# Performance work log

Hardware: AMD Instinct MI355X
Metric: run time of the kernel (lower is better)

The kernel has to match this reference:

```python
import jax, jax.numpy as jnp
import numpy as np

C, F, CLS, B, HW = 2048, 512, 200, 128, 14
SCALES = (4, 5, 7, 11)
EPS = 1e-5

def _pool_matrix(n, k):
    # PyTorch AdaptiveAvgPool2d bin edges: [floor(i*n/k), ceil((i+1)*n/k))
    P = np.zeros((k, n), np.float32)
    for i in range(k):
        s = (i * n) // k
        e = -((-(i + 1) * n) // k)
        P[i, s:e] = 1.0 / (e - s)
    return jnp.asarray(P)

_PMATS = [_pool_matrix(HW, k) for k in SCALES]

def _bn(x, g, b):
    # BatchNorm with batch statistics (train-mode), biased variance, eps=1e-5
    m = x.mean(0)
    v = x.var(0)
    return (x - m) * jax.lax.rsqrt(v + EPS) * g + b

def _head(h, g1, b1, w1, bi1, g2, b2, w2, bi2):
    # Sequential(BN, Linear, BN, ELU, Linear)
    h = _bn(h, g1, b1) @ w1.T + bi1
    h = jax.nn.elu(_bn(h, g2, b2))
    return h @ w2.T + bi2

def setup_inputs():
    key = jax.random.key(0)
    ks = iter(jax.random.split(key, 16))
    def rn(shape, scale=0.02):
        return jax.random.normal(next(ks), shape, jnp.float32) * scale
    d = {"x": jax.random.normal(next(ks), (B, C, HW, HW), jnp.float32)}
    d.update(g_bn_g=jnp.ones((C,)), g_bn_b=jnp.zeros((C,)), g_w=rn((4, C)), g_b=jnp.zeros((4,)))
    d.update(e_w=rn((C, C)), e_b=jnp.zeros((C,)), e_g=jnp.ones((C,)), e_bb=jnp.zeros((C,)))
    def head(p, din, dh):
        d[p + "_g1"] = jnp.ones((din,)); d[p + "_b1"] = jnp.zeros((din,))
        d[p + "_w1"] = rn((dh, din));   d[p + "_bi1"] = jnp.zeros((dh,))
        d[p + "_g2"] = jnp.ones((dh,)); d[p + "_b2"] = jnp.zeros((dh,))
        d[p + "_w2"] = rn((CLS, dh));   d[p + "_bi2"] = jnp.zeros((CLS,))
    head("hl", C, F)
    head("hh", C, F)
    head("hf", 2 * C, 2 * F)
    return d

def reference(x, g_bn_g, g_bn_b, g_w, g_b, e_w, e_b, e_g, e_bb,
              hl_g1, hl_b1, hl_w1, hl_bi1, hl_g2, hl_b2, hl_w2, hl_bi2,
              hh_g1, hh_b1, hh_w1, hh_bi1, hh_g2, hh_b2, hh_w2, hh_bi2,
              hf_g1, hf_b1, hf_w1, hf_bi1, hf_g2, hf_b2, hf_w2, hf_bi2):
    # Gate: global max pool -> BN -> ELU -> Linear -> hard gumbel-softmax (temp=1,
    # deterministic/eval: straight-through hard argmax over softmax)
    mp = x.max((2, 3))                                              # [B,C]
    logits = jax.nn.elu(_bn(mp, g_bn_g, g_bn_b)) @ g_w.T + g_b      # [B,4]
    soft = jax.nn.softmax(logits, -1)
    hard = jax.nn.one_hot(jnp.argmax(soft, -1), 4, dtype=soft.dtype)
    gw = jax.lax.stop_gradient(hard - soft) + soft                  # [B,4]
    # multi-scale adaptive avg pool (4,5,7,11) then global max per scale — fully batched
    ms = jnp.stack([jnp.einsum('ki,bcij,lj->bckl', P, x, P).max((2, 3)) for P in _PMATS], -1)  # [B,C,4]
    pool = jnp.einsum('bcs,bs->bc', ms, gw)                         # gated weighted sum
    # expert_low: 1x1 conv on 1x1 spatial == linear, then BN2d(batch stats) + ReLU
    xl = jax.nn.relu(_bn(pool @ e_w.T + e_b, e_g, e_bb))
    # NOTE: source computes expert_high(x) then overwrites with self.max(x) -> x_high = global max pool of x
    xh = mp
    xf = jnp.concatenate([xl, xh], -1)
    out_low = _head(xl, hl_g1, hl_b1, hl_w1, hl_bi1, hl_g2, hl_b2, hl_w2, hl_bi2)
    out_high = _head(xh, hh_g1, hh_b1, hh_w1, hh_bi1, hh_g2, hh_b2, hh_w2, hh_bi2)
    out = _head(xf, hf_g1, hf_b1, hf_w1, hf_bi1, hf_g2, hf_b2, hf_w2, hf_bi2)
    return (out_low, out_high, out)
```

## Files before the change

kernel.cpp:

```cpp
#include <hip/hip_runtime.h>
#include <math.h>

#define B_DIM 128
#define C_DIM 2048
#define HW2   196

typedef __attribute__((ext_vector_type(8))) short bf16x8;
typedef __attribute__((ext_vector_type(4))) float f32x4;

__device__ __forceinline__ unsigned short f2bf(float f) {
  unsigned u = __float_as_uint(f);
  u += 0x7FFFu + ((u >> 16) & 1u);
  return (unsigned short)(u >> 16);
}

__global__ __launch_bounds__(256) void pool_max_kernel(
    const float* __restrict__ x, float* __restrict__ mp, float* __restrict__ ms) {
  __shared__ float lds[4][4][208];
  const int tid  = threadIdx.x;
  const int w    = tid >> 6;
  const int lane = tid & 63;
  const int g    = lane >> 4;
  const int c    = lane & 15;
  const size_t waveBase = (size_t)blockIdx.x * 16 + w * 4;

  const float* src = x + waveBase * HW2;
  #pragma unroll
  for (int j = 0; j < 4; ++j) {
    int f = lane + 64 * j;
    if (f < 196) {
      int t = (f * 669) >> 15;
      float4 v = *(const float4*)(src + f * 4);
      *(float4*)&lds[w][t][(f - 49 * t) * 4] = v;
    }
  }

  float xv[14];
  const float* col = &lds[w][g][c];
  #pragma unroll
  for (int r = 0; r < 14; ++r) xv[r] = col[r * 14];

  float cmax = (c < 14) ? xv[0] : -INFINITY;
  #pragma unroll
  for (int r = 1; r < 14; ++r) if (c < 14) cmax = fmaxf(cmax, xv[r]);
  #pragma unroll
  for (int off = 8; off > 0; off >>= 1) cmax = fmaxf(cmax, __shfl_xor(cmax, off));

  float P[15];
  P[0] = 0.f;
  #pragma unroll
  for (int r = 0; r < 14; ++r) P[r + 1] = P[r] + xv[r];

  float sm0, sm1, sm2, sm3;

  {
    constexpr int rs[4] = {0, 3, 7, 10}, re[4] = {4, 7, 11, 14};
    const bool valid = (0x489u >> c) & 1;
    float vmax = -INFINITY;
    #pragma unroll
    for (int i = 0; i < 4; ++i) {
      float v  = P[re[i]] - P[rs[i]];
      float w2 = v + __shfl_down(v, 1);
      float w4 = w2 + __shfl_down(w2, 2);
      vmax = fmaxf(vmax, valid ? w4 : -INFINITY);
    }
    #pragma unroll
    for (int off = 8; off > 0; off >>= 1) vmax = fmaxf(vmax, __shfl_xor(vmax, off));
    sm0 = vmax * 0.0625f;
  }
  {
    constexpr int rs[5] = {0, 2, 5, 8, 11}, re[5] = {3, 6, 9, 12, 14};
    constexpr float srl[5] = {1.f/3.f, 0.25f, 0.25f, 0.25f, 1.f/3.f};
    const bool valid = (0x925u >> c) & 1;
    const bool is3   = (0x801u >> c) & 1;
    const float invc = is3 ? (1.f/3.f) : 0.25f;
    float vmax = -INFINITY;
    #pragma unroll
    for (int i = 0; i < 5; ++i) {
      float v  = P[re[i]] - P[rs[i]];
      float d1 = __shfl_down(v, 1);
      float d2 = __shfl_down(v, 2);
      float w2 = v + d1;
      float w3 = w2 + d2;
      float w4 = w2 + __shfl_down(w2, 2);
      float wv = (is3 ? w3 : w4) * invc * srl[i];
      vmax = fmaxf(vmax, valid ? wv : -INFINITY);
    }
    #pragma unroll
    for (int off = 8; off > 0; off >>= 1) vmax = fmaxf(vmax, __shfl_xor(vmax, off));
    sm1 = vmax;
  }
  {
    constexpr int rs[7] = {0, 2, 4, 6, 8, 10, 12};
    const bool valid = (0x1555u >> c) & 1;
    float vmax = -INFINITY;
    #pragma unroll
    for (int i = 0; i < 7; ++i) {
      float v  = P[rs[i] + 2] - P[rs[i]];
      float w2 = v + __shfl_down(v, 1);
      vmax = fmaxf(vmax, valid ? w2 : -INFINITY);
    }
    #pragma unroll
    for (int off = 8; off > 0; off >>= 1) vmax = fmaxf(vmax, __shfl_xor(vmax, off));
    sm2 = vmax * 0.25f;
  }
  {
    constexpr int rs[11] = {0, 1, 2, 3, 5, 6, 7, 8, 10, 11, 12};
    constexpr int re[11] = {2, 3, 4, 6, 7, 8, 9, 11, 12, 13, 14};
    constexpr float srl[11] = {0.5f, 0.5f, 0.5f, 1.f/3.f, 0.5f, 0.5f, 0.5f,
                               1.f/3.f, 0.5f, 0.5f, 0.5f};
    const bool valid = (0x1DEFu >> c) & 1;
    const bool is3   = (0x108u >> c) & 1;
    const float invc = is3 ? (1.f/3.f) : 0.5f;
    float vmax = -INFINITY;
    #pragma unroll
    for (int i = 0; i < 11; ++i) {
      float v  = P[re[i]] - P[rs[i]];
      float d1 = __shfl_down(v, 1);
      float d2 = __shfl_down(v, 2);
      float w2 = v + d1;
      float w3 = w2 + d2;
      float wv = (is3 ? w3 : w2) * invc * srl[i];
      vmax = fmaxf(vmax, valid ? wv : -INFINITY);
    }
    #pragma unroll
    for (int off = 8; off > 0; off >>= 1) vmax = fmaxf(vmax, __shfl_xor(vmax, off));
    sm3 = vmax;
  }

  if (c == 0) {
    size_t T = waveBase + g;
    mp[T] = cmax;
    *(float4*)&ms[T * 4] = make_float4(sm0, sm1, sm2, sm3);
  }
}

__global__ __launch_bounds__(256) void statsmp_kernel(
    const float* __restrict__ mp,
    const float* __restrict__ hh_g1, const float* __restrict__ hh_b1,
    const float* __restrict__ hf_g1, const float* __restrict__ hf_b1,
    float* __restrict__ mean_mp, float* __restrict__ rstd_mp,
    float* __restrict__ s_h, float* __restrict__ t_h,
    float* __restrict__ sf2, float* __restrict__ tf2) {
  const int ci = threadIdx.x & 15;
  const int g  = threadIdx.x >> 4;
  const int c  = blockIdx.x * 16 + ci;
  float s = 0.f, q = 0.f;
  #pragma unroll
  for (int r = 0; r < 8; ++r) {
    float v = mp[(size_t)(g * 8 + r) * C_DIM + c];
    s += v; q += v * v;
  }
  __shared__ float ss[16][16], qq[16][16];
  ss[g][ci] = s; qq[g][ci] = q;
  __syncthreads();
  if (g == 0) {
    float S = 0.f, Q = 0.f;
    #pragma unroll
    for (int j = 0; j < 16; ++j) { S += ss[j][ci]; Q += qq[j][ci]; }
    float m = S * (1.f / B_DIM);
    float var = Q * (1.f / B_DIM) - m * m;
    if (var < 0.f) var = 0.f;
    float r = rsqrtf(var + 1e-5f);
    mean_mp[c] = m; rstd_mp[c] = r;
    float a = r * hh_g1[c];        s_h[c] = a; t_h[c] = hh_b1[c] - m * a;
    float b = r * hf_g1[2048 + c]; sf2[c] = b; tf2[c] = hf_b1[2048 + c] - m * b;
  }
}

__global__ void gate_select_kernel(
    const float* __restrict__ mp,
    const float* __restrict__ mean, const float* __restrict__ rstd,
    const float* __restrict__ gg, const float* __restrict__ gb,
    const float* __restrict__ gw, const float* __restrict__ gbias,
    const float* __restrict__ ms, float* __restrict__ pool) {
  const int b = blockIdx.x;
  const int t = threadIdx.x;
  float s0 = 0.f, s1 = 0.f, s2 = 0.f, s3 = 0.f;
  for (int c = t; c < C_DIM; c += 256) {
    float v = mp[(size_t)b * C_DIM + c];
    float xn = (v - mean[c]) * rstd[c] * gg[c] + gb[c];
    float e = xn > 0.f ? xn : expm1f(xn);
    s0 += e * gw[c];
    s1 += e * gw[C_DIM + c];
    s2 += e * gw[2 * C_DIM + c];
    s3 += e * gw[3 * C_DIM + c];
  }
  __shared__ float red[4][256];
  __shared__ int ssel;
  red[0][t] = s0; red[1][t] = s1; red[2][t] = s2; red[3][t] = s3;
  __syncthreads();
  for (int st = 128; st > 0; st >>= 1) {
    if (t < st) {
      red[0][t] += red[0][t + st];
      red[1][t] += red[1][t + st];
      red[2][t] += red[2][t + st];
      red[3][t] += red[3][t + st];
    }
    __syncthreads();
  }
  if (t == 0) {
    float best = red[0][0] + gbias[0];
    int bi = 0;
    for (int j = 1; j < 4; ++j) {
      float l = red[j][0] + gbias[j];
      if (l > best) { best = l; bi = j; }
    }
    ssel = bi;
  }
  __syncthreads();
  const int sel = ssel;
  for (int c = t; c < C_DIM; c += 256)
    pool[(size_t)b * C_DIM + c] = ms[((size_t)b * C_DIM + c) * 4 + sel];
}

__global__ __launch_bounds__(256) void gemm_e_mfma_kernel(
    const float* __restrict__ A, const float* __restrict__ W,
    float* __restrict__ P) {
  __shared__ __align__(16) short As[128 * 64];
  __shared__ __align__(16) short Bs[64 * 64];
  const int t = threadIdx.x;
  const int n0 = blockIdx.x << 6;
  const int kbeg = blockIdx.y << 8;

  const int rowA = t >> 1, koffA = (t & 1) << 5;
  const int rowB = t >> 2, koffB = (t & 3) << 4;

  const int lane = t & 63, wav = t >> 6;
  const int r = lane & 15, kb = lane >> 4;
  int aoff[2][2], boff[2][4];
  #pragma unroll
  for (int kk = 0; kk < 2; ++kk) {
    #pragma unroll
    for (int mi = 0; mi < 2; ++mi) {
      int row = wav * 32 + mi * 16 + r;
      aoff[kk][mi] = row * 128 + ((((kk << 2) + kb) ^ (row & 7)) << 4);
    }
    #pragma unroll
    for (int ni = 0; ni < 4; ++ni) {
      int cl = ni * 16 + r;
      boff[kk][ni] = cl * 128 + ((((kk << 2) + kb) ^ (cl & 7)) << 4);
    }
  }

  f32x4 acc[2][4];
  #pragma unroll
  for (int mi = 0; mi < 2; ++mi)
    #pragma unroll
    for (int ni = 0; ni < 4; ++ni)
      acc[mi][ni] = (f32x4){0.f, 0.f, 0.f, 0.f};

  for (int kt = 0; kt < 256; kt += 64) {
    const int kg = kbeg + kt;
    const float4* ap = (const float4*)&A[(size_t)rowA * 2048 + kg + koffA];
    const float4* bp = (const float4*)&W[(size_t)(n0 + rowB) * 2048 + kg + koffB];
    float4 fa[8], fb[4];
    #pragma unroll
    for (int j = 0; j < 8; ++j) fa[j] = ap[j];
    #pragma unroll
    for (int j = 0; j < 4; ++j) fb[j] = bp[j];
    __syncthreads();
    #pragma unroll
    for (int j = 0; j < 4; ++j) {
      bf16x8 v;
      v[0] = (short)f2bf(fa[2*j].x);   v[1] = (short)f2bf(fa[2*j].y);
      v[2] = (short)f2bf(fa[2*j].z);   v[3] = (short)f2bf(fa[2*j].w);
      v[4] = (short)f2bf(fa[2*j+1].x); v[5] = (short)f2bf(fa[2*j+1].y);
      v[6] = (short)f2bf(fa[2*j+1].z); v[7] = (short)f2bf(fa[2*j+1].w);
      int slot = (koffA >> 3) + j;
      *(bf16x8*)((char*)As + rowA * 128 + ((slot ^ (rowA & 7)) << 4)) = v;
    }
    #pragma unroll
    for (int j = 0; j < 2; ++j) {
      bf16x8 v;
      v[0] = (short)f2bf(fb[2*j].x);   v[1] = (short)f2bf(fb[2*j].y);
      v[2] = (short)f2bf(fb[2*j].z);   v[3] = (short)f2bf(fb[2*j].w);
      v[4] = (short)f2bf(fb[2*j+1].x); v[5] = (short)f2bf(fb[2*j+1].y);
      v[6] = (short)f2bf(fb[2*j+1].z); v[7] = (short)f2bf(fb[2*j+1].w);
      int slot = (koffB >> 3) + j;
      *(bf16x8*)((char*)Bs + rowB * 128 + ((slot ^ (rowB & 7)) << 4)) = v;
    }
    __syncthreads();
    #pragma unroll
    for (int kk = 0; kk < 2; ++kk) {
      bf16x8 a0 = *(bf16x8*)((char*)As + aoff[kk][0]);
      bf16x8 a1 = *(bf16x8*)((char*)As + aoff[kk][1]);
      bf16x8 b0 = *(bf16x8*)((char*)Bs + boff[kk][0]);
      bf16x8 b1 = *(bf16x8*)((char*)Bs + boff[kk][1]);
      bf16x8 b2 = *(bf16x8*)((char*)Bs + boff[kk][2]);
      bf16x8 b3 = *(bf16x8*)((char*)Bs + boff[kk][3]);
      acc[0][0] = __builtin_amdgcn_mfma_f32_16x16x32_bf16(a0, b0, acc[0][0], 0, 0, 0);
      acc[0][1] = __builtin_amdgcn_mfma_f32_16x16x32_bf16(a0, b1, acc[0][1], 0, 0, 0);
      acc[0][2] = __builtin_amdgcn_mfma_f32_16x16x32_bf16(a0, b2, acc[0][2], 0, 0, 0);
      acc[0][3] = __builtin_amdgcn_mfma_f32_16x16x32_bf16(a0, b3, acc[0][3], 0, 0, 0);
      acc[1][0] = __builtin_amdgcn_mfma_f32_16x16x32_bf16(a1, b0, acc[1][0], 0, 0, 0);
      acc[1][1] = __builtin_amdgcn_mfma_f32_16x16x32_bf16(a1, b1, acc[1][1], 0, 0, 0);
      acc[1][2] = __builtin_amdgcn_mfma_f32_16x16x32_bf16(a1, b2, acc[1][2], 0, 0, 0);
      acc[1][3] = __builtin_amdgcn_mfma_f32_16x16x32_bf16(a1, b3, acc[1][3], 0, 0, 0);
    }
  }

  float* Pz = P + ((size_t)blockIdx.y << 18);
  #pragma unroll
  for (int mi = 0; mi < 2; ++mi) {
    int row = wav * 32 + mi * 16 + kb * 4;
    #pragma unroll
    for (int ni = 0; ni < 4; ++ni) {
      int cl = n0 + ni * 16 + r;
      #pragma unroll
      for (int g2 = 0; g2 < 4; ++g2)
        Pz[(size_t)(row + g2) * 2048 + cl] = acc[mi][ni][g2];
    }
  }
}

__global__ __launch_bounds__(256) void expert_fused_kernel(
    const float* __restrict__ Pe, const float* __restrict__ e_b,
    const float* __restrict__ e_g, const float* __restrict__ e_bb,
    const float* __restrict__ hl_g1, const float* __restrict__ hl_b1,
    const float* __restrict__ hf_g1, const float* __restrict__ hf_b1,
    float* __restrict__ xl,
    float* __restrict__ s_l, float* __restrict__ t_l,
    float* __restrict__ sf1, float* __restrict__ tf1) {
  const int ci = threadIdx.x & 15;
  const int g  = threadIdx.x >> 4;
  const int c  = blockIdx.x * 16 + ci;
  float v[8];
  float s = 0.f, q = 0.f;
  const float bias = e_b[c];
  #pragma unroll
  for (int r = 0; r < 8; ++r) {
    const size_t row = g * 8 + r;
    float acc = bias;
    #pragma unroll
    for (int z = 0; z < 8; ++z)
      acc += Pe[((size_t)z << 18) + row * 2048 + c];
    v[r] = acc; s += acc; q += acc * acc;
  }
  __shared__ float ss[16][16], qq[16][16];
  __shared__ float sm[16], sr[16];
  ss[g][ci] = s; qq[g][ci] = q;
  __syncthreads();
  if (g == 0) {
    float S = 0.f, Q = 0.f;
    #pragma unroll
    for (int j = 0; j < 16; ++j) { S += ss[j][ci]; Q += qq[j][ci]; }
    float m = S * (1.f / B_DIM);
    float var = Q * (1.f / B_DIM) - m * m;
    if (var < 0.f) var = 0.f;
    sm[ci] = m; sr[ci] = rsqrtf(var + 1e-5f);
  }
  __syncthreads();
  const float m = sm[ci], rst = sr[ci];
  const float eg = e_g[c], eb2 = e_bb[c];
  float s2 = 0.f, q2 = 0.f;
  #pragma unroll
  for (int r = 0; r < 8; ++r) {
    float xv = fmaxf((v[r] - m) * rst * eg + eb2, 0.f);
    xl[(size_t)(g * 8 + r) * 2048 + c] = xv;
    s2 += xv; q2 += xv * xv;
  }
  __syncthreads();
  ss[g][ci] = s2; qq[g][ci] = q2;
  __syncthreads();
  if (g == 0) {
    float S = 0.f, Q = 0.f;
    #pragma unroll
    for (int j = 0; j < 16; ++j) { S += ss[j][ci]; Q += qq[j][ci]; }
    float mm = S * (1.f / B_DIM);
    float var = Q * (1.f / B_DIM) - mm * mm;
    if (var < 0.f) var = 0.f;
    float rr = rsqrtf(var + 1e-5f);
    float a = rr * hl_g1[c]; s_l[c] = a; t_l[c] = hl_b1[c] - mm * a;
    float b = rr * hf_g1[c]; sf1[c] = b; tf1[c] = hf_b1[c] - mm * b;
  }
}

__global__ __launch_bounds__(256) void gemm_w1_mfma_kernel(
    const float* __restrict__ xl, const float* __restrict__ mp,
    const float* __restrict__ s_l, const float* __restrict__ t_l,
    const float* __restrict__ s_h, const float* __restrict__ t_h,
    const float* __restrict__ sf1, const float* __restrict__ tf1,
    const float* __restrict__ sf2, const float* __restrict__ tf2,
    const float* __restrict__ hl_w1, const float* __restrict__ hh_w1,
    const float* __restrict__ hf_w1,
    float* __restrict__ P_l, float* __restrict__ P_h, float* __restrict__ P_f) {
  __shared__ __align__(16) short As[128 * 64];
  __shared__ __align__(16) short Bs[64 * 64];
  const int jx = blockIdx.x;
  const int z  = blockIdx.y;
  const float *A, *S, *T, *Wt;
  float* P;
  int N, Kdim, n0, kA0, kW0, Kc;
  if (jx < 8) {
    N = 512; Kdim = 2048; Kc = 128; Wt = hl_w1; n0 = jx << 6;
    kW0 = z * 128; kA0 = kW0; A = xl; S = s_l; T = t_l;
    P = P_l + ((size_t)z << 16);
  } else if (jx < 16) {
    N = 512; Kdim = 2048; Kc = 128; Wt = hh_w1; n0 = (jx - 8) << 6;
    kW0 = z * 128; kA0 = kW0; A = mp; S = s_h; T = t_h;
    P = P_h + ((size_t)z << 16);
  } else {
    N = 1024; Kdim = 4096; Kc = 256; Wt = hf_w1; n0 = (jx - 16) << 6;
    kW0 = z * 256;
    if (kW0 >= 2048) { A = mp; S = sf2; T = tf2; kA0 = kW0 - 2048; }
    else             { A = xl; S = sf1; T = tf1; kA0 = kW0; }
    P = P_f + ((size_t)z << 17);
  }
  const int t = threadIdx.x;
  const int rowA = t >> 1, koffA = (t & 1) << 5;
  const int rowB = t >> 2, koffB = (t & 3) << 4;

  const int lane = t & 63, wav = t >> 6;
  const int r = lane & 15, kb = lane >> 4;
  int aoff[2][2], boff[2][4];
  #pragma unroll
  for (int kk = 0; kk < 2; ++kk) {
    #pragma unroll
    for (int mi = 0; mi < 2; ++mi) {
      int row = wav * 32 + mi * 16 + r;
      aoff[kk][mi] = row * 128 + ((((kk << 2) + kb) ^ (row & 7)) << 4);
    }
    #pragma unroll
    for (int ni = 0; ni < 4; ++ni) {
      int cl = ni * 16 + r;
      boff[kk][ni] = cl * 128 + ((((kk << 2) + kb) ^ (cl & 7)) << 4);
    }
  }

  f32x4 acc[2][4];
  #pragma unroll
  for (int mi = 0; mi < 2; ++mi)
    #pragma unroll
    for (int ni = 0; ni < 4; ++ni)
      acc[mi][ni] = (f32x4){0.f, 0.f, 0.f, 0.f};

  for (int kt = 0; kt < Kc; kt += 64) {
    const int ka = kA0 + kt + koffA;
    const float4* ap = (const float4*)&A[(size_t)rowA * 2048 + ka];
    const float4* sp = (const float4*)&S[ka];
    const float4* tp = (const float4*)&T[ka];
    const float4* bp = (const float4*)&Wt[(size_t)(n0 + rowB) * Kdim + kW0 + kt + koffB];
    float4 fa[8], fb[4];
    #pragma unroll
    for (int j = 0; j < 8; ++j) fa[j] = ap[j];
    #pragma unroll
    for (int j = 0; j < 8; ++j) {
      float4 s4 = sp[j], t4 = tp[j];
      fa[j].x = fmaf(fa[j].x, s4.x, t4.x);
      fa[j].y = fmaf(fa[j].y, s4.y, t4.y);
      fa[j].z = fmaf(fa[j].z, s4.z, t4.z);
      fa[j].w = fmaf(fa[j].w, s4.w, t4.w);
    }
    #pragma unroll
    for (int j = 0; j < 4; ++j) fb[j] = bp[j];
    __syncthreads();
    #pragma unroll
    for (int j = 0; j < 4; ++j) {
      bf16x8 v;
      v[0] = (short)f2bf(fa[2*j].x);   v[1] = (short)f2bf(fa[2*j].y);
      v[2] = (short)f2bf(fa[2*j].z);   v[3] = (short)f2bf(fa[2*j].w);
      v[4] = (short)f2bf(fa[2*j+1].x); v[5] = (short)f2bf(fa[2*j+1].y);
      v[6] = (short)f2bf(fa[2*j+1].z); v[7] = (short)f2bf(fa[2*j+1].w);
      int slot = (koffA >> 3) + j;
      *(bf16x8*)((char*)As + rowA * 128 + ((slot ^ (rowA & 7)) << 4)) = v;
    }
    #pragma unroll
    for (int j = 0; j < 2; ++j) {
      bf16x8 v;
      v[0] = (short)f2bf(fb[2*j].x);   v[1] = (short)f2bf(fb[2*j].y);
      v[2] = (short)f2bf(fb[2*j].z);   v[3] = (short)f2bf(fb[2*j].w);
      v[4] = (short)f2bf(fb[2*j+1].x); v[5] = (short)f2bf(fb[2*j+1].y);
      v[6] = (short)f2bf(fb[2*j+1].z); v[7] = (short)f2bf(fb[2*j+1].w);
      int slot = (koffB >> 3) + j;
      *(bf16x8*)((char*)Bs + rowB * 128 + ((slot ^ (rowB & 7)) << 4)) = v;
    }
    __syncthreads();
    #pragma unroll
    for (int kk = 0; kk < 2; ++kk) {
      bf16x8 a0 = *(bf16x8*)((char*)As + aoff[kk][0]);
      bf16x8 a1 = *(bf16x8*)((char*)As + aoff[kk][1]);
      bf16x8 b0 = *(bf16x8*)((char*)Bs + boff[kk][0]);
      bf16x8 b1 = *(bf16x8*)((char*)Bs + boff[kk][1]);
      bf16x8 b2 = *(bf16x8*)((char*)Bs + boff[kk][2]);
      bf16x8 b3 = *(bf16x8*)((char*)Bs + boff[kk][3]);
      acc[0][0] = __builtin_amdgcn_mfma_f32_16x16x32_bf16(a0, b0, acc[0][0], 0, 0, 0);
      acc[0][1] = __builtin_amdgcn_mfma_f32_16x16x32_bf16(a0, b1, acc[0][1], 0, 0, 0);
      acc[0][2] = __builtin_amdgcn_mfma_f32_16x16x32_bf16(a0, b2, acc[0][2], 0, 0, 0);
      acc[0][3] = __builtin_amdgcn_mfma_f32_16x16x32_bf16(a0, b3, acc[0][3], 0, 0, 0);
      acc[1][0] = __builtin_amdgcn_mfma_f32_16x16x32_bf16(a1, b0, acc[1][0], 0, 0, 0);
      acc[1][1] = __builtin_amdgcn_mfma_f32_16x16x32_bf16(a1, b1, acc[1][1], 0, 0, 0);
      acc[1][2] = __builtin_amdgcn_mfma_f32_16x16x32_bf16(a1, b2, acc[1][2], 0, 0, 0);
      acc[1][3] = __builtin_amdgcn_mfma_f32_16x16x32_bf16(a1, b3, acc[1][3], 0, 0, 0);
    }
  }

  #pragma unroll
  for (int mi = 0; mi < 2; ++mi) {
    int row = wav * 32 + mi * 16 + kb * 4;
    #pragma unroll
    for (int ni = 0; ni < 4; ++ni) {
      int cl = n0 + ni * 16 + r;
      #pragma unroll
      for (int g2 = 0; g2 < 4; ++g2)
        P[(size_t)(row + g2) * N + cl] = acc[mi][ni][g2];
    }
  }
}

__global__ __launch_bounds__(256) void heads_fused_kernel(
    const float* __restrict__ P_l, const float* __restrict__ P_h,
    const float* __restrict__ P_f,
    const float* __restrict__ bl1, const float* __restrict__ bh1,
    const float* __restrict__ bf1,
    const float* __restrict__ g2l, const float* __restrict__ b2l,
    const float* __restrict__ g2h, const float* __restrict__ b2h,
    const float* __restrict__ g2f, const float* __restrict__ b2f,
    float* __restrict__ a2_l, float* __restrict__ a2_h, float* __restrict__ a2_f) {
  const int ci = threadIdx.x & 15;
  const int g  = threadIdx.x >> 4;
  const int cj = blockIdx.x * 16 + ci;
  const float *P, *bi, *g2, *b2;
  float* out;
  int N, cc;
  if (cj < 512)       { P = P_l; bi = bl1; g2 = g2l; b2 = b2l; out = a2_l; N = 512;  cc = cj; }
  else if (cj < 1024) { P = P_h; bi = bh1; g2 = g2h; b2 = b2h; out = a2_h; N = 512;  cc = cj - 512; }
  else                { P = P_f; bi = bf1; g2 = g2f; b2 = b2f; out = a2_f; N = 1024; cc = cj - 1024; }
  const size_t sstride = (size_t)N * 128;
  float v[8];
  float s = 0.f, q = 0.f;
  const float bias = bi[cc];
  #pragma unroll
  for (int r = 0; r < 8; ++r) {
    const size_t row = g * 8 + r;
    float acc = bias;
    #pragma unroll
    for (int z = 0; z < 16; ++z)
      acc += P[(size_t)z * sstride + row * N + cc];
    v[r] = acc; s += acc; q += acc * acc;
  }
  __shared__ float ss[16][16], qq[16][16];
  __shared__ float sm[16], sr[16];
  ss[g][ci] = s; qq[g][ci] = q;
  __syncthreads();
  if (g == 0) {
    float S = 0.f, Q = 0.f;
    #pragma unroll
    for (int j = 0; j < 16; ++j) { S += ss[j][ci]; Q += qq[j][ci]; }
    float m = S * (1.f / B_DIM);
    float var = Q * (1.f / B_DIM) - m * m;
    if (var < 0.f) var = 0.f;
    sm[ci] = m; sr[ci] = rsqrtf(var + 1e-5f);
  }
  __syncthreads();
  const float m = sm[ci], rr = sr[ci];
  const float gg = g2[cc], bb = b2[cc];
  #pragma unroll
  for (int r = 0; r < 8; ++r) {
    float xn = (v[r] - m) * rr * gg + bb;
    out[(size_t)(g * 8 + r) * N + cc] = xn > 0.f ? xn : expm1f(xn);
  }
}

__global__ __launch_bounds__(256) void gemm_w2_kernel(
    const float* __restrict__ a2_l, const float* __restrict__ a2_h,
    const float* __restrict__ a2_f,
    const float* __restrict__ hl_w2, const float* __restrict__ hh_w2,
    const float* __restrict__ hf_w2,
    float* __restrict__ Pw) {
  const int jx = blockIdx.x;
  const int z  = blockIdx.z;
  const float *A, *Wt;
  int K, Kc, pOff, n0;
  if (jx < 4)      { A = a2_l; Wt = hl_w2; K = 512;  Kc = 64;  pOff = 0;     n0 = jx << 6; }
  else if (jx < 8) { A = a2_h; Wt = hh_w2; K = 512;  Kc = 64;  pOff = 25600; n0 = (jx - 4) << 6; }
  else             { A = a2_f; Wt = hf_w2; K = 1024; Kc = 128; pOff = 51200; n0 = (jx - 8) << 6; }
  const int kbeg = z * Kc;
  const int m0 = blockIdx.y << 6;
  __shared__ float As[32][68];
  __shared__ float Bs[32][68];
  const int t = threadIdx.x;
  const int lr = t >> 3;
  const int lk4 = (t & 7) << 2;
  const int tx = t & 15, ty = t >> 4;
  float acc[4][4] = {{0.f}};
  const float4 z4 = make_float4(0.f, 0.f, 0.f, 0.f);
  for (int k0 = kbeg; k0 < kbeg + Kc; k0 += 32) {
    float4 a0 = *(const float4*)&A[(size_t)(m0 + lr) * K + k0 + lk4];
    float4 a1 = *(const float4*)&A[(size_t)(m0 + lr + 32) * K + k0 + lk4];
    int n1 = n0 + lr, n2 = n0 + lr + 32;
    float4 b0 = (n1 < 200) ? *(const float4*)&Wt[(size_t)n1 * K + k0 + lk4] : z4;
    float4 b1 = (n2 < 200) ? *(const float4*)&Wt[(size_t)n2 * K + k0 + lk4] : z4;
    __syncthreads();
    As[lk4 + 0][lr] = a0.x; As[lk4 + 1][lr] = a0.y; As[lk4 + 2][lr] = a0.z; As[lk4 + 3][lr] = a0.w;
    As[lk4 + 0][lr + 32] = a1.x; As[lk4 + 1][lr + 32] = a1.y; As[lk4 + 2][lr + 32] = a1.z; As[lk4 + 3][lr + 32] = a1.w;
    Bs[lk4 + 0][lr] = b0.x; Bs[lk4 + 1][lr] = b0.y; Bs[lk4 + 2][lr] = b0.z; Bs[lk4 + 3][lr] = b0.w;
    Bs[lk4 + 0][lr + 32] = b1.x; Bs[lk4 + 1][lr + 32] = b1.y; Bs[lk4 + 2][lr + 32] = b1.z; Bs[lk4 + 3][lr + 32] = b1.w;
    __syncthreads();
    #pragma unroll
    for (int kk = 0; kk < 32; ++kk) {
      float4 av = *(const float4*)&As[kk][ty << 2];
      float4 bv = *(const float4*)&Bs[kk][tx << 2];
      acc[0][0] = fmaf(av.x, bv.x, acc[0][0]); acc[0][1] = fmaf(av.x, bv.y, acc[0][1]);
      acc[0][2] = fmaf(av.x, bv.z, acc[0][2]); acc[0][3] = fmaf(av.x, bv.w, acc[0][3]);
      acc[1][0] = fmaf(av.y, bv.x, acc[1][0]); acc[1][1] = fmaf(av.y, bv.y, acc[1][1]);
      acc[1][2] = fmaf(av.y, bv.z, acc[1][2]); acc[1][3] = fmaf(av.y, bv.w, acc[1][3]);
      acc[2][0] = fmaf(av.z, bv.x, acc[2][0]); acc[2][1] = fmaf(av.z, bv.y, acc[2][1]);
      acc[2][2] = fmaf(av.z, bv.z, acc[2][2]); acc[2][3] = fmaf(av.z, bv.w, acc[2][3]);
      acc[3][0] = fmaf(av.w, bv.x, acc[3][0]); acc[3][1] = fmaf(av.w, bv.y, acc[3][1]);
      acc[3][2] = fmaf(av.w, bv.z, acc[3][2]); acc[3][3] = fmaf(av.w, bv.w, acc[3][3]);
    }
  }
  float* Pz = Pw + (size_t)z * 76800 + pOff;
  #pragma unroll
  for (int i = 0; i < 4; ++i) {
    int m = m0 + (ty << 2) + i;
    #pragma unroll
    for (int j = 0; j < 4; ++j) {
      int n = n0 + (tx << 2) + j;
      if (n < 200) Pz[(size_t)m * 200 + n] = acc[i][j];
    }
  }
}

__global__ void reduce_out_kernel(const float* __restrict__ P,
                                  const float* __restrict__ bl,
                                  const float* __restrict__ bh,
                                  const float* __restrict__ bf,
                                  float* __restrict__ out) {
  int i = blockIdx.x * 256 + threadIdx.x;
  if (i >= 76800) return;
  int job = i / 25600;
  int n = (i - job * 25600) % 200;
  float s = (job == 0) ? bl[n] : (job == 1) ? bh[n] : bf[n];
  for (int z = 0; z < 8; ++z) s += P[(size_t)z * 76800 + i];
  out[i] = s;
}

extern "C" void kernel_launch(void* const* d_in, const int* in_sizes, int n_in,
                              void* d_out, int out_size, void* d_ws, size_t ws_size,
                              hipStream_t stream) {
  const float* x      = (const float*)d_in[0];
  const float* g_bn_g = (const float*)d_in[1];
  const float* g_bn_b = (const float*)d_in[2];
  const float* g_w    = (const float*)d_in[3];
  const float* g_b    = (const float*)d_in[4];
  const float* e_w    = (const float*)d_in[5];
  const float* e_b    = (const float*)d_in[6];
  const float* e_g    = (const float*)d_in[7];
  const float* e_bb   = (const float*)d_in[8];
  const float* hl_g1  = (const float*)d_in[9];
  const float* hl_b1  = (const float*)d_in[10];
  const float* hl_w1  = (const float*)d_in[11];
  const float* hl_bi1 = (const float*)d_in[12];
  const float* hl_g2  = (const float*)d_in[13];
  const float* hl_b2  = (const float*)d_in[14];
  const float* hl_w2  = (const float*)d_in[15];
  const float* hl_bi2 = (const float*)d_in[16];
  const float* hh_g1  = (const float*)d_in[17];
  const float* hh_b1  = (const float*)d_in[18];
  const float* hh_w1  = (const float*)d_in[19];
  const float* hh_bi1 = (const float*)d_in[20];
  const float* hh_g2  = (const float*)d_in[21];
  const float* hh_b2  = (const float*)d_in[22];
  const float* hh_w2  = (const float*)d_in[23];
  const float* hh_bi2 = (const float*)d_in[24];
  const float* hf_g1  = (const float*)d_in[25];
  const float* hf_b1  = (const float*)d_in[26];
  const float* hf_w1  = (const float*)d_in[27];
  const float* hf_bi1 = (const float*)d_in[28];
  const float* hf_g2  = (const float*)d_in[29];
  const float* hf_b2  = (const float*)d_in[30];
  const float* hf_w2  = (const float*)d_in[31];
  const float* hf_bi2 = (const float*)d_in[32];
  float* out = (float*)d_out;

  float* W = (float*)d_ws;
  const size_t BC = (size_t)B_DIM * C_DIM;
  float* mp   = W;
  float* ms   = mp + BC;
  float* pool = ms + BC * 4;
  float* xl   = pool + BC;
  float* a2_l = xl + BC;
  float* a2_h = a2_l + 128 * 512;
  float* a2_f = a2_h + 128 * 512;
  float* st   = a2_f + 128 * 1024;
  float* mean_mp = st;           float* rstd_mp = st + 2048;
  float* s_h  = st + 2 * 2048;   float* t_h  = st + 3 * 2048;
  float* sf2  = st + 4 * 2048;   float* tf2  = st + 5 * 2048;
  float* s_l  = st + 6 * 2048;   float* t_l  = st + 7 * 2048;
  float* sf1  = st + 8 * 2048;   float* tf1  = st + 9 * 2048;
  float* P_e  = st + 10 * 2048;
  float* P_l2 = P_e + 8 * BC;
  float* P_hh = P_l2 + (size_t)16 * 65536;
  float* P_f  = P_hh + (size_t)16 * 65536;
  float* P_w2 = P_e;

  pool_max_kernel<<<16384, 256, 0, stream>>>(x, mp, ms);

  statsmp_kernel<<<128, 256, 0, stream>>>(mp, hh_g1, hh_b1, hf_g1, hf_b1,
                                          mean_mp, rstd_mp, s_h, t_h, sf2, tf2);

  gate_select_kernel<<<128, 256, 0, stream>>>(mp, mean_mp, rstd_mp, g_bn_g, g_bn_b,
                                              g_w, g_b, ms, pool);

  gemm_e_mfma_kernel<<<dim3(32, 8), 256, 0, stream>>>(pool, e_w, P_e);

  expert_fused_kernel<<<128, 256, 0, stream>>>(P_e, e_b, e_g, e_bb,
                                               hl_g1, hl_b1, hf_g1, hf_b1,
                                               xl, s_l, t_l, sf1, tf1);

  gemm_w1_mfma_kernel<<<dim3(32, 16), 256, 0, stream>>>(
      xl, mp, s_l, t_l, s_h, t_h, sf1, tf1, sf2, tf2,
      hl_w1, hh_w1, hf_w1, P_l2, P_hh, P_f);

  heads_fused_kernel<<<128, 256, 0, stream>>>(
      P_l2, P_hh, P_f, hl_bi1, hh_bi1, hf_bi1,
      hl_g2, hl_b2, hh_g2, hh_b2, hf_g2, hf_b2,
      a2_l, a2_h, a2_f);

  gemm_w2_kernel<<<dim3(12, 2, 8), 256, 0, stream>>>(
      a2_l, a2_h, a2_f, hl_w2, hh_w2, hf_w2, P_w2);

  reduce_out_kernel<<<300, 256, 0, stream>>>(P_w2, hl_bi2, hh_bi2, hf_bi2, out);
}
```

Baseline: 139.5 us.

## Use MFMA for final head GEMM, drop split-K reduce, halve W1 split-K

```diff
diff --git a/kernel.cpp b/kernel.cpp
--- a/kernel.cpp
+++ b/kernel.cpp
@@ -30,8 +30,8 @@
     int f = lane + 64 * j;
     if (f < 196) {
       int t = (f * 669) >> 15;
-      float4 v = *(const float4*)(src + f * 4);
-      *(float4*)&lds[w][t][(f - 49 * t) * 4] = v;
+      f32x4 v = __builtin_nontemporal_load((const f32x4*)(src + f * 4));
+      *(f32x4*)&lds[w][t][(f - 49 * t) * 4] = v;
     }
   }
 
@@ -393,16 +393,16 @@
   float* P;
   int N, Kdim, n0, kA0, kW0, Kc;
   if (jx < 8) {
-    N = 512; Kdim = 2048; Kc = 128; Wt = hl_w1; n0 = jx << 6;
-    kW0 = z * 128; kA0 = kW0; A = xl; S = s_l; T = t_l;
+    N = 512; Kdim = 2048; Kc = 256; Wt = hl_w1; n0 = jx << 6;
+    kW0 = z * 256; kA0 = kW0; A = xl; S = s_l; T = t_l;
     P = P_l + ((size_t)z << 16);
   } else if (jx < 16) {
-    N = 512; Kdim = 2048; Kc = 128; Wt = hh_w1; n0 = (jx - 8) << 6;
-    kW0 = z * 128; kA0 = kW0; A = mp; S = s_h; T = t_h;
+    N = 512; Kdim = 2048; Kc = 256; Wt = hh_w1; n0 = (jx - 8) << 6;
+    kW0 = z * 256; kA0 = kW0; A = mp; S = s_h; T = t_h;
     P = P_h + ((size_t)z << 16);
   } else {
-    N = 1024; Kdim = 4096; Kc = 256; Wt = hf_w1; n0 = (jx - 16) << 6;
-    kW0 = z * 256;
+    N = 1024; Kdim = 4096; Kc = 512; Wt = hf_w1; n0 = (jx - 16) << 6;
+    kW0 = z * 512;
     if (kW0 >= 2048) { A = mp; S = sf2; T = tf2; kA0 = kW0 - 2048; }
     else             { A = xl; S = sf1; T = tf1; kA0 = kW0; }
     P = P_f + ((size_t)z << 17);
@@ -535,7 +535,7 @@
     const size_t row = g * 8 + r;
     float acc = bias;
     #pragma unroll
-    for (int z = 0; z < 16; ++z)
+    for (int z = 0; z < 8; ++z)
       acc += P[(size_t)z * sstride + row * N + cc];
     v[r] = acc; s += acc; q += acc * acc;
   }
@@ -562,79 +562,123 @@
   }
 }
 
-__global__ __launch_bounds__(256) void gemm_w2_kernel(
+__global__ __launch_bounds__(256) void gemm_w2_mfma_kernel(
     const float* __restrict__ a2_l, const float* __restrict__ a2_h,
     const float* __restrict__ a2_f,
     const float* __restrict__ hl_w2, const float* __restrict__ hh_w2,
     const float* __restrict__ hf_w2,
-    float* __restrict__ Pw) {
+    const float* __restrict__ bl2, const float* __restrict__ bh2,
+    const float* __restrict__ bf2,
+    float* __restrict__ out) {
+  __shared__ __align__(16) short As[128 * 64];
+  __shared__ __align__(16) short Bs[64 * 64];
   const int jx = blockIdx.x;
-  const int z  = blockIdx.z;
-  const float *A, *Wt;
-  int K, Kc, pOff, n0;
-  if (jx < 4)      { A = a2_l; Wt = hl_w2; K = 512;  Kc = 64;  pOff = 0;     n0 = jx << 6; }
-  else if (jx < 8) { A = a2_h; Wt = hh_w2; K = 512;  Kc = 64;  pOff = 25600; n0 = (jx - 4) << 6; }
-  else             { A = a2_f; Wt = hf_w2; K = 1024; Kc = 128; pOff = 51200; n0 = (jx - 8) << 6; }
-  const int kbeg = z * Kc;
-  const int m0 = blockIdx.y << 6;
-  __shared__ float As[32][68];
-  __shared__ float Bs[32][68];
+  const float *A, *Wt, *bi;
+  int K, outOff;
+  if (jx < 4)      { A = a2_l; Wt = hl_w2; bi = bl2; K = 512;  outOff = 0; }
+  else if (jx < 8) { A = a2_h; Wt = hh_w2; bi = bh2; K = 512;  outOff = 25600; }
+  else             { A = a2_f; Wt = hf_w2; bi = bf2; K = 1024; outOff = 51200; }
+  const int n0 = (jx & 3) << 6;
+
   const int t = threadIdx.x;
-  const int lr = t >> 3;
-  const int lk4 = (t & 7) << 2;
-  const int tx = t & 15, ty = t >> 4;
-  float acc[4][4] = {{0.f}};
+  const int rowA = t >> 1, koffA = (t & 1) << 5;
+  const int rowB = t >> 2, koffB = (t & 3) << 4;
+
+  const int lane = t & 63, wav = t >> 6;
+  const int r = lane & 15, kb = lane >> 4;
+  int aoff[2][2], boff[2][4];
+  #pragma unroll
+  for (int kk = 0; kk < 2; ++kk) {
+    #pragma unroll
+    for (int mi = 0; mi < 2; ++mi) {
+      int row = wav * 32 + mi * 16 + r;
+      aoff[kk][mi] = row * 128 + ((((kk << 2) + kb) ^ (row & 7)) << 4);
+    }
+    #pragma unroll
+    for (int ni = 0; ni < 4; ++ni) {
+      int cl = ni * 16 + r;
+      boff[kk][ni] = cl * 128 + ((((kk << 2) + kb) ^ (cl & 7)) << 4);
+    }
+  }
+
+  f32x4 acc[2][4];
+  #pragma unroll
+  for (int mi = 0; mi < 2; ++mi)
+    #pragma unroll
+    for (int ni = 0; ni < 4; ++ni)
+      acc[mi][ni] = (f32x4){0.f, 0.f, 0.f, 0.f};
+
+  const int wrow = n0 + rowB;
   const float4 z4 = make_float4(0.f, 0.f, 0.f, 0.f);
-  for (int k0 = kbeg; k0 < kbeg + Kc; k0 += 32) {
-    float4 a0 = *(const float4*)&A[(size_t)(m0 + lr) * K + k0 + lk4];
-    float4 a1 = *(const float4*)&A[(size_t)(m0 + lr + 32) * K + k0 + lk4];
-    int n1 = n0 + lr, n2 = n0 + lr + 32;
-    float4 b0 = (n1 < 200) ? *(const float4*)&Wt[(size_t)n1 * K + k0 + lk4] : z4;
-    float4 b1 = (n2 < 200) ? *(const float4*)&Wt[(size_t)n2 * K + k0 + lk4] : z4;
+  for (int kt = 0; kt < K; kt += 64) {
+    const float4* ap = (const float4*)&A[(size_t)rowA * K + kt + koffA];
+    float4 fa[8], fb[4];
+    #pragma unroll
+    for (int j = 0; j < 8; ++j) fa[j] = ap[j];
+    if (wrow < 200) {
+      const float4* bp = (const float4*)&Wt[(size_t)wrow * K + kt + koffB];
+      #pragma unroll
+      for (int j = 0; j < 4; ++j) fb[j] = bp[j];
+    } else {
+      #pragma unroll
+      for (int j = 0; j < 4; ++j) fb[j] = z4;
+    }
     __syncthreads();
-    As[lk4 + 0][lr] = a0.x; As[lk4 + 1][lr] = a0.y; As[lk4 + 2][lr] = a0.z; As[lk4 + 3][lr] = a0.w;
-    As[lk4 + 0][lr + 32] = a1.x; As[lk4 + 1][lr + 32] = a1.y; As[lk4 + 2][lr + 32] = a1.z; As[lk4 + 3][lr + 32] = a1.w;
-    Bs[lk4 + 0][lr] = b0.x; Bs[lk4 + 1][lr] = b0.y; Bs[lk4 + 2][lr] = b0.z; Bs[lk4 + 3][lr] = b0.w;
-    Bs[lk4 + 0][lr + 32] = b1.x; Bs[lk4 + 1][lr + 32] = b1.y; Bs[lk4 + 2][lr + 32] = b1.z; Bs[lk4 + 3][lr + 32] = b1.w;
+    #pragma unroll
+    for (int j = 0; j < 4; ++j) {
+      bf16x8 v;
+      v[0] = (short)f2bf(fa[2*j].x);   v[1] = (short)f2bf(fa[2*j].y);
+      v[2] = (short)f2bf(fa[2*j].z);   v[3] = (short)f2bf(fa[2*j].w);
+      v[4] = (short)f2bf(fa[2*j+1].x); v[5] = (short)f2bf(fa[2*j+1].y);
+      v[6] = (short)f2bf(fa[2*j+1].z); v[7] = (short)f2bf(fa[2*j+1].w);
+      int slot = (koffA >> 3) + j;
+      *(bf16x8*)((char*)As + rowA * 128 + ((slot ^ (rowA & 7)) << 4)) = v;
+    }
+    #pragma unroll
+    for (int j = 0; j < 2; ++j) {
+      bf16x8 v;
+      v[0] = (short)f2bf(fb[2*j].x);   v[1] = (short)f2bf(fb[2*j].y);
+      v[2] = (short)f2bf(fb[2*j].z);   v[3] = (short)f2bf(fb[2*j].w);
+      v[4] = (short)f2bf(fb[2*j+1].x); v[5] = (short)f2bf(fb[2*j+1].y);
+      v[6] = (short)f2bf(fb[2*j+1].z); v[7] = (short)f2bf(fb[2*j+1].w);
+      int slot = (koffB >> 3) + j;
+      *(bf16x8*)((char*)Bs + rowB * 128 + ((slot ^ (rowB & 7)) << 4)) = v;
+    }
     __syncthreads();
     #pragma unroll
-    for (int kk = 0; kk < 32; ++kk) {
-      float4 av = *(const float4*)&As[kk][ty << 2];
-      float4 bv = *(const float4*)&Bs[kk][tx << 2];
-      acc[0][0] = fmaf(av.x, bv.x, acc[0][0]); acc[0][1] = fmaf(av.x, bv.y, acc[0][1]);
-      acc[0][2] = fmaf(av.x, bv.z, acc[0][2]); acc[0][3] = fmaf(av.x, bv.w, acc[0][3]);
-      acc[1][0] = fmaf(av.y, bv.x, acc[1][0]); acc[1][1] = fmaf(av.y, bv.y, acc[1][1]);
-      acc[1][2] = fmaf(av.y, bv.z, acc[1][2]); acc[1][3] = fmaf(av.y, bv.w, acc[1][3]);
-      acc[2][0] = fmaf(av.z, bv.x, acc[2][0]); acc[2][1] = fmaf(av.z, bv.y, acc[2][1]);
-      acc[2][2] = fmaf(av.z, bv.z, acc[2][2]); acc[2][3] = fmaf(av.z, bv.w, acc[2][3]);
-      acc[3][0] = fmaf(av.w, bv.x, acc[3][0]); acc[3][1] = fmaf(av.w, bv.y, acc[3][1]);
-      acc[3][2] = fmaf(av.w, bv.z, acc[3][2]); acc[3][3] = fmaf(av.w, bv.w, acc[3][3]);
-    }
-  }
-  float* Pz = Pw + (size_t)z * 76800 + pOff;
-  #pragma unroll
-  for (int i = 0; i < 4; ++i) {
-    int m = m0 + (ty << 2) + i;
-    #pragma unroll
-    for (int j = 0; j < 4; ++j) {
-      int n = n0 + (tx << 2) + j;
-      if (n < 200) Pz[(size_t)m * 200 + n] = acc[i][j];
-    }
-  }
-}
-
-__global__ void reduce_out_kernel(const float* __restrict__ P,
-                                  const float* __restrict__ bl,
-                                  const float* __restrict__ bh,
-                                  const float* __restrict__ bf,
-                                  float* __restrict__ out) {
-  int i = blockIdx.x * 256 + threadIdx.x;
-  if (i >= 76800) return;
-  int job = i / 25600;
-  int n = (i - job * 25600) % 200;
-  float s = (job == 0) ? bl[n] : (job == 1) ? bh[n] : bf[n];
-  for (int z = 0; z < 8; ++z) s += P[(size_t)z * 76800 + i];
-  out[i] = s;
+    for (int kk = 0; kk < 2; ++kk) {
+      bf16x8 a0 = *(bf16x8*)((char*)As + aoff[kk][0]);
+      bf16x8 a1 = *(bf16x8*)((char*)As + aoff[kk][1]);
+      bf16x8 b0 = *(bf16x8*)((char*)Bs + boff[kk][0]);
+      bf16x8 b1 = *(bf16x8*)((char*)Bs + boff[kk][1]);
+      bf16x8 b2 = *(bf16x8*)((char*)Bs + boff[kk][2]);
+      bf16x8 b3 = *(bf16x8*)((char*)Bs + boff[kk][3]);
+      acc[0][0] = __builtin_amdgcn_mfma_f32_16x16x32_bf16(a0, b0, acc[0][0], 0, 0, 0);
+      acc[0][1] = __builtin_amdgcn_mfma_f32_16x16x32_bf16(a0, b1, acc[0][1], 0, 0, 0);
+      acc[0][2] = __builtin_amdgcn_mfma_f32_16x16x32_bf16(a0, b2, acc[0][2], 0, 0, 0);
+      acc[0][3] = __builtin_amdgcn_mfma_f32_16x16x32_bf16(a0, b3, acc[0][3], 0, 0, 0);
+      acc[1][0] = __builtin_amdgcn_mfma_f32_16x16x32_bf16(a1, b0, acc[1][0], 0, 0, 0);
+      acc[1][1] = __builtin_amdgcn_mfma_f32_16x16x32_bf16(a1, b1, acc[1][1], 0, 0, 0);
+      acc[1][2] = __builtin_amdgcn_mfma_f32_16x16x32_bf16(a1, b2, acc[1][2], 0, 0, 0);
+      acc[1][3] = __builtin_amdgcn_mfma_f32_16x16x32_bf16(a1, b3, acc[1][3], 0, 0, 0);
+    }
+  }
+
+  float* O = out + outOff;
+  #pragma unroll
+  for (int mi = 0; mi < 2; ++mi) {
+    int row = wav * 32 + mi * 16 + kb * 4;
+    #pragma unroll
+    for (int ni = 0; ni < 4; ++ni) {
+      int cl = n0 + ni * 16 + r;
+      if (cl < 200) {
+        float bv = bi[cl];
+        #pragma unroll
+        for (int g2 = 0; g2 < 4; ++g2)
+          O[(size_t)(row + g2) * 200 + cl] = acc[mi][ni][g2] + bv;
+      }
+    }
+  }
 }
 
 extern "C" void kernel_launch(void* const* d_in, const int* in_sizes, int n_in,
@@ -692,9 +736,8 @@
   float* sf1  = st + 8 * 2048;   float* tf1  = st + 9 * 2048;
   float* P_e  = st + 10 * 2048;
   float* P_l2 = P_e + 8 * BC;
-  float* P_hh = P_l2 + (size_t)16 * 65536;
-  float* P_f  = P_hh + (size_t)16 * 65536;
-  float* P_w2 = P_e;
+  float* P_hh = P_l2 + (size_t)8 * 65536;
+  float* P_f  = P_hh + (size_t)8 * 65536;
 
   pool_max_kernel<<<16384, 256, 0, stream>>>(x, mp, ms);
 
@@ -710,7 +753,7 @@
                                                hl_g1, hl_b1, hf_g1, hf_b1,
                                                xl, s_l, t_l, sf1, tf1);
 
-  gemm_w1_mfma_kernel<<<dim3(32, 16), 256, 0, stream>>>(
+  gemm_w1_mfma_kernel<<<dim3(32, 8), 256, 0, stream>>>(
       xl, mp, s_l, t_l, s_h, t_h, sf1, tf1, sf2, tf2,
       hl_w1, hh_w1, hf_w1, P_l2, P_hh, P_f);
 
@@ -719,8 +762,7 @@
       hl_g2, hl_b2, hh_g2, hh_b2, hf_g2, hf_b2,
       a2_l, a2_h, a2_f);
 
-  gemm_w2_kernel<<<dim3(12, 2, 8), 256, 0, stream>>>(
-      a2_l, a2_h, a2_f, hl_w2, hh_w2, hf_w2, P_w2);
-
-  reduce_out_kernel<<<300, 256, 0, stream>>>(P_w2, hl_bi2, hh_bi2, hf_bi2, out);
-}
+  gemm_w2_mfma_kernel<<<12, 256, 0, stream>>>(
+      a2_l, a2_h, a2_f, hl_w2, hh_w2, hf_w2,
+      hl_bi2, hh_bi2, hf_bi2, out);
+}
```

Measured after the change: 157.2 us. 12.7% more time.

## Retile first-layer head GEMM to 64-row M tiles with halved split-K

Applied to the files above, without the earlier changes.

```diff
diff --git a/kernel.cpp b/kernel.cpp
--- a/kernel.cpp
+++ b/kernel.cpp
@@ -385,42 +385,39 @@
     const float* __restrict__ hl_w1, const float* __restrict__ hh_w1,
     const float* __restrict__ hf_w1,
     float* __restrict__ P_l, float* __restrict__ P_h, float* __restrict__ P_f) {
-  __shared__ __align__(16) short As[128 * 64];
+  __shared__ __align__(16) short As[64 * 64];
   __shared__ __align__(16) short Bs[64 * 64];
   const int jx = blockIdx.x;
-  const int z  = blockIdx.y;
+  const int m0 = blockIdx.y << 6;
+  const int z  = blockIdx.z;
   const float *A, *S, *T, *Wt;
   float* P;
   int N, Kdim, n0, kA0, kW0, Kc;
   if (jx < 8) {
-    N = 512; Kdim = 2048; Kc = 128; Wt = hl_w1; n0 = jx << 6;
-    kW0 = z * 128; kA0 = kW0; A = xl; S = s_l; T = t_l;
+    N = 512; Kdim = 2048; Kc = 256; Wt = hl_w1; n0 = jx << 6;
+    kW0 = z * 256; kA0 = kW0; A = xl; S = s_l; T = t_l;
     P = P_l + ((size_t)z << 16);
   } else if (jx < 16) {
-    N = 512; Kdim = 2048; Kc = 128; Wt = hh_w1; n0 = (jx - 8) << 6;
-    kW0 = z * 128; kA0 = kW0; A = mp; S = s_h; T = t_h;
+    N = 512; Kdim = 2048; Kc = 256; Wt = hh_w1; n0 = (jx - 8) << 6;
+    kW0 = z * 256; kA0 = kW0; A = mp; S = s_h; T = t_h;
     P = P_h + ((size_t)z << 16);
   } else {
-    N = 1024; Kdim = 4096; Kc = 256; Wt = hf_w1; n0 = (jx - 16) << 6;
-    kW0 = z * 256;
+    N = 1024; Kdim = 4096; Kc = 512; Wt = hf_w1; n0 = (jx - 16) << 6;
+    kW0 = z * 512;
     if (kW0 >= 2048) { A = mp; S = sf2; T = tf2; kA0 = kW0 - 2048; }
     else             { A = xl; S = sf1; T = tf1; kA0 = kW0; }
     P = P_f + ((size_t)z << 17);
   }
   const int t = threadIdx.x;
-  const int rowA = t >> 1, koffA = (t & 1) << 5;
-  const int rowB = t >> 2, koffB = (t & 3) << 4;
+  const int rowS = t >> 2, koff = (t & 3) << 4;
 
   const int lane = t & 63, wav = t >> 6;
   const int r = lane & 15, kb = lane >> 4;
-  int aoff[2][2], boff[2][4];
+  int aoff[2], boff[2][4];
   #pragma unroll
   for (int kk = 0; kk < 2; ++kk) {
-    #pragma unroll
-    for (int mi = 0; mi < 2; ++mi) {
-      int row = wav * 32 + mi * 16 + r;
-      aoff[kk][mi] = row * 128 + ((((kk << 2) + kb) ^ (row & 7)) << 4);
-    }
+    int row = wav * 16 + r;
+    aoff[kk] = row * 128 + ((((kk << 2) + kb) ^ (row & 7)) << 4);
     #pragma unroll
     for (int ni = 0; ni < 4; ++ni) {
       int cl = ni * 16 + r;
@@ -428,24 +425,21 @@
     }
   }
 
-  f32x4 acc[2][4];
-  #pragma unroll
-  for (int mi = 0; mi < 2; ++mi)
-    #pragma unroll
-    for (int ni = 0; ni < 4; ++ni)
-      acc[mi][ni] = (f32x4){0.f, 0.f, 0.f, 0.f};
+  f32x4 acc[4];
+  #pragma unroll
+  for (int ni = 0; ni < 4; ++ni) acc[ni] = (f32x4){0.f, 0.f, 0.f, 0.f};
 
   for (int kt = 0; kt < Kc; kt += 64) {
-    const int ka = kA0 + kt + koffA;
-    const float4* ap = (const float4*)&A[(size_t)rowA * 2048 + ka];
+    const int ka = kA0 + kt + koff;
+    const float4* ap = (const float4*)&A[(size_t)(m0 + rowS) * 2048 + ka];
     const float4* sp = (const float4*)&S[ka];
     const float4* tp = (const float4*)&T[ka];
-    const float4* bp = (const float4*)&Wt[(size_t)(n0 + rowB) * Kdim + kW0 + kt + koffB];
-    float4 fa[8], fb[4];
-    #pragma unroll
-    for (int j = 0; j < 8; ++j) fa[j] = ap[j];
-    #pragma unroll
-    for (int j = 0; j < 8; ++j) {
+    const float4* bp = (const float4*)&Wt[(size_t)(n0 + rowS) * Kdim + kW0 + kt + koff];
+    float4 fa[4], fb[4];
+    #pragma unroll
+    for (int j = 0; j < 4; ++j) fa[j] = ap[j];
+    #pragma unroll
+    for (int j = 0; j < 4; ++j) {
       float4 s4 = sp[j], t4 = tp[j];
       fa[j].x = fmaf(fa[j].x, s4.x, t4.x);
       fa[j].y = fmaf(fa[j].y, s4.y, t4.y);
@@ -456,55 +450,42 @@
     for (int j = 0; j < 4; ++j) fb[j] = bp[j];
     __syncthreads();
     #pragma unroll
-    for (int j = 0; j < 4; ++j) {
-      bf16x8 v;
-      v[0] = (short)f2bf(fa[2*j].x);   v[1] = (short)f2bf(fa[2*j].y);
-      v[2] = (short)f2bf(fa[2*j].z);   v[3] = (short)f2bf(fa[2*j].w);
-      v[4] = (short)f2bf(fa[2*j+1].x); v[5] = (short)f2bf(fa[2*j+1].y);
-      v[6] = (short)f2bf(fa[2*j+1].z); v[7] = (short)f2bf(fa[2*j+1].w);
-      int slot = (koffA >> 3) + j;
-      *(bf16x8*)((char*)As + rowA * 128 + ((slot ^ (rowA & 7)) << 4)) = v;
-    }
-    #pragma unroll
     for (int j = 0; j < 2; ++j) {
-      bf16x8 v;
-      v[0] = (short)f2bf(fb[2*j].x);   v[1] = (short)f2bf(fb[2*j].y);
-      v[2] = (short)f2bf(fb[2*j].z);   v[3] = (short)f2bf(fb[2*j].w);
-      v[4] = (short)f2bf(fb[2*j+1].x); v[5] = (short)f2bf(fb[2*j+1].y);
-      v[6] = (short)f2bf(fb[2*j+1].z); v[7] = (short)f2bf(fb[2*j+1].w);
-      int slot = (koffB >> 3) + j;
-      *(bf16x8*)((char*)Bs + rowB * 128 + ((slot ^ (rowB & 7)) << 4)) = v;
+      bf16x8 va, vb;
+      va[0] = (short)f2bf(fa[2*j].x);   va[1] = (short)f2bf(fa[2*j].y);
+      va[2] = (short)f2bf(fa[2*j].z);   va[3] = (short)f2bf(fa[2*j].w);
+      va[4] = (short)f2bf(fa[2*j+1].x); va[5] = (short)f2bf(fa[2*j+1].y);
+      va[6] = (short)f2bf(fa[2*j+1].z); va[7] = (short)f2bf(fa[2*j+1].w);
+      vb[0] = (short)f2bf(fb[2*j].x);   vb[1] = (short)f2bf(fb[2*j].y);
+      vb[2] = (short)f2bf(fb[2*j].z);   vb[3] = (short)f2bf(fb[2*j].w);
+      vb[4] = (short)f2bf(fb[2*j+1].x); vb[5] = (short)f2bf(fb[2*j+1].y);
+      vb[6] = (short)f2bf(fb[2*j+1].z); vb[7] = (short)f2bf(fb[2*j+1].w);
+      int slot = (koff >> 3) + j;
+      *(bf16x8*)((char*)As + rowS * 128 + ((slot ^ (rowS & 7)) << 4)) = va;
+      *(bf16x8*)((char*)Bs + rowS * 128 + ((slot ^ (rowS & 7)) << 4)) = vb;
     }
     __syncthreads();
     #pragma unroll
     for (int kk = 0; kk < 2; ++kk) {
-      bf16x8 a0 = *(bf16x8*)((char*)As + aoff[kk][0]);
-      bf16x8 a1 = *(bf16x8*)((char*)As + aoff[kk][1]);
+      bf16x8 a0 = *(bf16x8*)((char*)As + aoff[kk]);
       bf16x8 b0 = *(bf16x8*)((char*)Bs + boff[kk][0]);
       bf16x8 b1 = *(bf16x8*)((char*)Bs + boff[kk][1]);
       bf16x8 b2 = *(bf16x8*)((char*)Bs + boff[kk][2]);
       bf16x8 b3 = *(bf16x8*)((char*)Bs + boff[kk][3]);
-      acc[0][0] = __builtin_amdgcn_mfma_f32_16x16x32_bf16(a0, b0, acc[0][0], 0, 0, 0);
-      acc[0][1] = __builtin_amdgcn_mfma_f32_16x16x32_bf16(a0, b1, acc[0][1], 0, 0, 0);
-      acc[0][2] = __builtin_amdgcn_mfma_f32_16x16x32_bf16(a0, b2, acc[0][2], 0, 0, 0);
-      acc[0][3] = __builtin_amdgcn_mfma_f32_16x16x32_bf16(a0, b3, acc[0][3], 0, 0, 0);
-      acc[1][0] = __builtin_amdgcn_mfma_f32_16x16x32_bf16(a1, b0, acc[1][0], 0, 0, 0);
-      acc[1][1] = __builtin_amdgcn_mfma_f32_16x16x32_bf16(a1, b1, acc[1][1], 0, 0, 0);
-      acc[1][2] = __builtin_amdgcn_mfma_f32_16x16x32_bf16(a1, b2, acc[1][2], 0, 0, 0);
-      acc[1][3] = __builtin_amdgcn_mfma_f32_16x16x32_bf16(a1, b3, acc[1][3], 0, 0, 0);
-    }
-  }
-
-  #pragma unroll
-  for (int mi = 0; mi < 2; ++mi) {
-    int row = wav * 32 + mi * 16 + kb * 4;
-    #pragma unroll
-    for (int ni = 0; ni < 4; ++ni) {
-      int cl = n0 + ni * 16 + r;
-      #pragma unroll
-      for (int g2 = 0; g2 < 4; ++g2)
-        P[(size_t)(row + g2) * N + cl] = acc[mi][ni][g2];
-    }
+      acc[0] = __builtin_amdgcn_mfma_f32_16x16x32_bf16(a0, b0, acc[0], 0, 0, 0);
+      acc[1] = __builtin_amdgcn_mfma_f32_16x16x32_bf16(a0, b1, acc[1], 0, 0, 0);
+      acc[2] = __builtin_amdgcn_mfma_f32_16x16x32_bf16(a0, b2, acc[2], 0, 0, 0);
+      acc[3] = __builtin_amdgcn_mfma_f32_16x16x32_bf16(a0, b3, acc[3], 0, 0, 0);
+    }
+  }
+
+  #pragma unroll
+  for (int ni = 0; ni < 4; ++ni) {
+    int cl = n0 + ni * 16 + r;
+    int row = m0 + wav * 16 + kb * 4;
+    #pragma unroll
+    for (int g2 = 0; g2 < 4; ++g2)
+      P[(size_t)(row + g2) * N + cl] = acc[ni][g2];
   }
 }
 
@@ -535,7 +516,7 @@
     const size_t row = g * 8 + r;
     float acc = bias;
     #pragma unroll
-    for (int z = 0; z < 16; ++z)
+    for (int z = 0; z < 8; ++z)
       acc += P[(size_t)z * sstride + row * N + cc];
     v[r] = acc; s += acc; q += acc * acc;
   }
@@ -692,8 +673,8 @@
   float* sf1  = st + 8 * 2048;   float* tf1  = st + 9 * 2048;
   float* P_e  = st + 10 * 2048;
   float* P_l2 = P_e + 8 * BC;
-  float* P_hh = P_l2 + (size_t)16 * 65536;
-  float* P_f  = P_hh + (size_t)16 * 65536;
+  float* P_hh = P_l2 + (size_t)8 * 65536;
+  float* P_f  = P_hh + (size_t)8 * 65536;
   float* P_w2 = P_e;
 
   pool_max_kernel<<<16384, 256, 0, stream>>>(x, mp, ms);
@@ -710,7 +691,7 @@
                                                hl_g1, hl_b1, hf_g1, hf_b1,
                                                xl, s_l, t_l, sf1, tf1);
 
-  gemm_w1_mfma_kernel<<<dim3(32, 16), 256, 0, stream>>>(
+  gemm_w1_mfma_kernel<<<dim3(32, 2, 8), 256, 0, stream>>>(
       xl, mp, s_l, t_l, s_h, t_h, sf1, tf1, sf2, tf2,
       hl_w1, hh_w1, hf_w1, P_l2, P_hh, P_f);
 
```

Result: faster. 131.7 us (-5.6%).
